# Kernel tuning notes

Hardware: AMD Instinct MI355X
Metric: run time of the kernel (lower is better)

## Reference

```python
import jax, jax.numpy as jnp
import numpy as np

D_MODEL = 1024
NUM_HEADS = 16
HEAD_DIM = D_MODEL // NUM_HEADS
B, T = 4, 2048


def setup_inputs() -> dict:
    key = jax.random.key(0)
    ks = jax.random.split(key, 6)
    s = 1.0 / np.sqrt(D_MODEL)  # ~ nn.Linear init scale
    return {
        "x_q": jax.random.normal(ks[0], (B, T, D_MODEL), jnp.float32),
        "x_kv": jax.random.normal(ks[1], (B, T, D_MODEL), jnp.float32),
        "Wq": jax.random.uniform(ks[2], (D_MODEL, D_MODEL), jnp.float32, -s, s),
        "Wk": jax.random.uniform(ks[3], (D_MODEL, D_MODEL), jnp.float32, -s, s),
        "Wv": jax.random.uniform(ks[4], (D_MODEL, D_MODEL), jnp.float32, -s, s),
        "Wo": jax.random.uniform(ks[5], (D_MODEL, D_MODEL), jnp.float32, -s, s),
    }


def reference(x_q, x_kv, Wq, Wk, Wv, Wo):
    Bq, Tq, C = x_q.shape
    Tk = x_kv.shape[1]
    # torch nn.Linear: y = x @ W.T
    q = (x_q @ Wq.T).reshape(Bq, Tq, NUM_HEADS, HEAD_DIM).transpose(0, 2, 1, 3)
    k = (x_kv @ Wk.T).reshape(Bq, Tk, NUM_HEADS, HEAD_DIM).transpose(0, 2, 1, 3)
    v = (x_kv @ Wv.T).reshape(Bq, Tk, NUM_HEADS, HEAD_DIM).transpose(0, 2, 1, 3)
    scores = jnp.einsum("bhqd,bhkd->bhqk", q, k) / jnp.sqrt(
        jnp.asarray(HEAD_DIM, x_q.dtype)
    )
    causal = jnp.triu(jnp.ones((Tq, Tk), bool), k=1)  # True above diagonal
    scores = jnp.where(causal, -jnp.inf, scores)
    attn = jax.nn.softmax(scores, axis=-1)
    out = jnp.einsum("bhqk,bhkd->bhqd", attn, v)
    out = out.transpose(0, 2, 1, 3).reshape(Bq, Tq, C)
    return out @ Wo.T
```

## Files before the change

kernel.cpp:

```cpp
#include <hip/hip_runtime.h>
#include <stdint.h>

#define T_SEQ 2048
#define NH 16
#define HD 64
#define DM 1024
#define BB 4
#define MROWS (BB * T_SEQ)

#define QSCALE 0.18033688011112042f

typedef __attribute__((ext_vector_type(8))) __bf16 bf16x8;
typedef __attribute__((ext_vector_type(8))) unsigned short u16x8;
typedef __attribute__((ext_vector_type(4))) unsigned short u16x4;
typedef __attribute__((ext_vector_type(4))) float f32x4;

__device__ __forceinline__ unsigned short f2bf(float f) {
  return __builtin_bit_cast(unsigned short, (__bf16)f);
}

__device__ __forceinline__ bf16x8 ld8_f32(const float* __restrict__ p) {
  f32x4 a = *(const f32x4*)p;
  f32x4 b = *(const f32x4*)(p + 4);
  u16x8 u;
#pragma unroll
  for (int i = 0; i < 4; ++i) {
    u[i]     = f2bf(a[i]);
    u[i + 4] = f2bf(b[i]);
  }
  return __builtin_bit_cast(bf16x8, u);
}

__device__ __forceinline__ bf16x8 ld8_bf(const unsigned short* p) {
  return __builtin_bit_cast(bf16x8, *(const u16x8*)p);
}

__device__ __forceinline__ bf16x8 ld8_lds(const unsigned short* p) {
  u16x4 a = *(const u16x4*)p;
  u16x4 b = *(const u16x4*)(p + 4);
  return __builtin_bit_cast(bf16x8,
      __builtin_shufflevector(a, b, 0, 1, 2, 3, 4, 5, 6, 7));
}

__device__ __forceinline__ u16x4 lo4(u16x8 v) {
  return __builtin_shufflevector(v, v, 0, 1, 2, 3);
}
__device__ __forceinline__ u16x4 hi4(u16x8 v) {
  return __builtin_shufflevector(v, v, 4, 5, 6, 7);
}

__device__ __forceinline__ void gload_lds16(const unsigned short* g,
                                            unsigned short* l) {
  __builtin_amdgcn_global_load_lds(
      (const __attribute__((address_space(1))) unsigned int*)g,
      (__attribute__((address_space(3))) unsigned int*)l, 16, 0, 0);
}

__global__ __launch_bounds__(256) void conv_f32_bf16(
    const float* __restrict__ src, unsigned short* __restrict__ dst, int n8) {
  const int i = blockIdx.x * 256 + threadIdx.x;
  if (i < n8)
    *(u16x8*)(dst + (size_t)i * 8) =
        __builtin_bit_cast(u16x8, ld8_f32(src + (size_t)i * 8));
}

__global__ __launch_bounds__(256) void conv_stage1(
    const float* __restrict__ Wk, const float* __restrict__ Wv,
    const float* __restrict__ Wq, const float* __restrict__ Wo,
    const float* __restrict__ xkv, unsigned short* __restrict__ Wkb012,
    unsigned short* __restrict__ Wob, unsigned short* __restrict__ Sx) {
  const int bid = blockIdx.x;
  const int WSEG = (DM * DM / 8) / 256;
  if (bid < 4 * WSEG) {
    const int w = bid >> 9;
    const float* src = (w == 0) ? Wk : (w == 1) ? Wv : (w == 2) ? Wq : Wo;
    unsigned short* dst = (w < 3) ? Wkb012 + (size_t)w * DM * DM : Wob;
    const int i = (bid & (WSEG - 1)) * 256 + threadIdx.x;
    *(u16x8*)(dst + (size_t)i * 8) =
        __builtin_bit_cast(u16x8, ld8_f32(src + (size_t)i * 8));
  } else {
    const int i = (bid - 4 * WSEG) * 256 + threadIdx.x;
    *(u16x8*)(Sx + (size_t)i * 8) =
        __builtin_bit_cast(u16x8, ld8_f32(xkv + (size_t)i * 8));
  }
}

template <int MODE>
__global__ __launch_bounds__(256) void gemm128(
    const unsigned short* __restrict__ A, const unsigned short* __restrict__ B,
    void* __restrict__ Cv, void* __restrict__ Cv2, int M, int N, int K) {
  __shared__ __align__(16) unsigned short As[2][2][128 * 32];
  __shared__ __align__(16) unsigned short Bs[2][2][128 * 32];

  const int t = threadIdx.x;
  const int lane = t & 63, wave = t >> 6;
  const int lin = (int)(blockIdx.x + gridDim.x * blockIdx.y);
  const int nx = N >> 7;
  const int mpx = (M >> 7) >> 3;
  const int xcd = lin & 7, slot = lin >> 3;
  const int m0 = (xcd * mpx + slot / nx) * 128;
  const int n0 = (slot % nx) * 128;

  const int srow = t >> 2;
  const int scol = (t & 3) * 8;
  const unsigned short* ga0 = A + (size_t)(m0 + srow) * K + scol;
  const unsigned short* ga1 = A + (size_t)(m0 + 64 + srow) * K + scol;
  const unsigned short* gb0 = B + (size_t)(n0 + srow) * K + scol;
  const unsigned short* gb1 = B + (size_t)(n0 + 64 + srow) * K + scol;
  const int lo0 = (wave * 16) * 32, lo1 = (64 + wave * 16) * 32;

  const int mw = (wave >> 1) * 64, nw = (wave & 1) * 64;
  const int fr = lane & 15, fq = (lane >> 4) * 8;

  f32x4 acc[4][4];
#pragma unroll
  for (int i = 0; i < 4; ++i)
#pragma unroll
    for (int j = 0; j < 4; ++j) acc[i][j] = (f32x4){0.f, 0.f, 0.f, 0.f};

  auto stage = [&](int buf, int k0) {
    gload_lds16(ga0 + k0,      &As[buf][0][lo0]);
    gload_lds16(ga1 + k0,      &As[buf][0][lo1]);
    gload_lds16(gb0 + k0,      &Bs[buf][0][lo0]);
    gload_lds16(gb1 + k0,      &Bs[buf][0][lo1]);
    gload_lds16(ga0 + k0 + 32, &As[buf][1][lo0]);
    gload_lds16(ga1 + k0 + 32, &As[buf][1][lo1]);
    gload_lds16(gb0 + k0 + 32, &Bs[buf][1][lo0]);
    gload_lds16(gb1 + k0 + 32, &Bs[buf][1][lo1]);
  };

  stage(0, 0);
  __syncthreads();

  const int NT = K >> 6;
  int cur = 0;
  for (int kt = 0; kt < NT; ++kt) {
    if (kt + 1 < NT) stage(cur ^ 1, (kt + 1) << 6);
#pragma unroll
    for (int ks = 0; ks < 2; ++ks) {
      bf16x8 af[4], bfr[4];
#pragma unroll
      for (int i = 0; i < 4; ++i)
        af[i] = ld8_bf(&As[cur][ks][(mw + i * 16 + fr) * 32 + fq]);
#pragma unroll
      for (int j = 0; j < 4; ++j)
        bfr[j] = ld8_bf(&Bs[cur][ks][(nw + j * 16 + fr) * 32 + fq]);
#pragma unroll
      for (int i = 0; i < 4; ++i)
#pragma unroll
        for (int j = 0; j < 4; ++j)
          acc[i][j] = __builtin_amdgcn_mfma_f32_16x16x32_bf16(
              af[i], bfr[j], acc[i][j], 0, 0, 0);
    }
    __syncthreads();
    cur ^= 1;
  }

  const int orow = (lane >> 4) * 4, ocol = lane & 15;
  const bool kv_lo = (MODE == 3) && (n0 < DM);
#pragma unroll
  for (int i = 0; i < 4; ++i)
#pragma unroll
    for (int j = 0; j < 4; ++j) {
      if constexpr (MODE == 2) {
        const int mb = m0 + mw + i * 16 + orow;
        const int n = n0 + nw + j * 16 + ocol;
        u16x4 pk;
#pragma unroll
        for (int r = 0; r < 4; ++r) pk[r] = f2bf(acc[i][j][r]);
        unsigned short* dst = (unsigned short*)Cv +
            ((size_t)((mb >> 11) * NH + (n >> 6)) * HD + (n & 63)) * T_SEQ +
            (mb & 2047);
        *(u16x4*)dst = pk;
      } else if constexpr (MODE == 3) {
        const int mb = m0 + mw + i * 16 + orow;
        const int n = n0 + nw + j * 16 + ocol;
        if (kv_lo) {
#pragma unroll
          for (int r = 0; r < 4; ++r)
            ((unsigned short*)Cv)[(size_t)(mb + r) * DM + n] =
                f2bf(acc[i][j][r]);
        } else {
          const int nv = n - DM;
          u16x4 pk;
#pragma unroll
          for (int r = 0; r < 4; ++r) pk[r] = f2bf(acc[i][j][r]);
          unsigned short* dst = (unsigned short*)Cv2 +
              ((size_t)((mb >> 11) * NH + (nv >> 6)) * HD + (nv & 63)) *
                  T_SEQ +
              (mb & 2047);
          *(u16x4*)dst = pk;
        }
      } else {
#pragma unroll
        for (int r = 0; r < 4; ++r) {
          const size_t idx = (size_t)(m0 + mw + i * 16 + orow + r) * N +
                             (n0 + nw + j * 16 + ocol);
          float v = acc[i][j][r];
          if constexpr (MODE == 4) v *= QSCALE;
          if constexpr (MODE == 1)
            ((float*)Cv)[idx] = v;
          else
            ((unsigned short*)Cv)[idx] = f2bf(v);
        }
      }
    }
}

#define ASTR 68

__global__ __launch_bounds__(256, 2) void attn_flash2(
    const unsigned short* Qw, const unsigned short* __restrict__ Kw,
    const unsigned short* __restrict__ Vt, unsigned short* Ow) {
  __shared__ __align__(16) unsigned short k_lds[2][64][ASTR];
  __shared__ __align__(16) unsigned short vt_lds[2][64][ASTR];
  __shared__ __align__(16) unsigned short p_lds[4][32][ASTR];

  const int tid = threadIdx.x, lane = tid & 63, wave = tid >> 6;
  const int c16 = lane & 15, quad = lane >> 4;
  const int b = blockIdx.z, h = blockIdx.y;
  const int pi = blockIdx.x;
  const int qb0A = (15 - pi) * 128;
  const int qb0B = pi * 128;
  const size_t rkbase = (size_t)b * T_SEQ * DM + (size_t)h * HD;
  const size_t vtbase = (size_t)(b * NH + h) * HD * T_SEQ;

  const int q_loA = qb0A + wave * 32;
  const int q_loB = qb0B + wave * 32;

  bf16x8 qfA[2][2], qfB[2][2];
#pragma unroll
  for (int nf = 0; nf < 2; ++nf) {
    const unsigned short* qpA =
        Qw + rkbase + (size_t)(q_loA + nf * 16 + c16) * DM + quad * 8;
    qfA[nf][0] = ld8_bf(qpA);
    qfA[nf][1] = ld8_bf(qpA + 32);
    const unsigned short* qpB =
        Qw + rkbase + (size_t)(q_loB + nf * 16 + c16) * DM + quad * 8;
    qfB[nf][0] = ld8_bf(qpB);
    qfB[nf][1] = ld8_bf(qpB + 32);
  }

  f32x4 oA[2][4], oB[2][4];
#pragma unroll
  for (int nf = 0; nf < 2; ++nf)
#pragma unroll
    for (int j = 0; j < 4; ++j) {
      oA[nf][j] = (f32x4){0.f, 0.f, 0.f, 0.f};
      oB[nf][j] = (f32x4){0.f, 0.f, 0.f, 0.f};
    }
  float mA[2] = {-3.0e38f, -3.0e38f}, lA[2] = {0.f, 0.f};
  float mB[2] = {-3.0e38f, -3.0e38f}, lB[2] = {0.f, 0.f};

  const int srow = tid >> 2;
  const int scol = (tid & 3) * 16;
  const int ntiles = (qb0A + 191) >> 6;
  const int ntA_w = (q_loA + 95) >> 6;
  const int ntB_w = (q_loB + 95) >> 6;

  const unsigned short* kp0 = Kw + rkbase + (size_t)srow * DM + scol;
  const unsigned short* vp0 = Vt + vtbase + (size_t)srow * T_SEQ + scol;

  auto subtile = [&](const bf16x8 (&qf)[2][2], f32x4 (&o)[2][4],
                     float (&m_r)[2], float (&l_r)[2], const int q_lo,
                     const int kb0, const int bi) {
    f32x4 s[4][2];
    __builtin_amdgcn_s_setprio(1);
#pragma unroll
    for (int mf = 0; mf < 4; ++mf) {
      const unsigned short* kr = &k_lds[bi][mf * 16 + c16][quad * 8];
      const bf16x8 k0 = ld8_lds(kr);
      const bf16x8 k1 = ld8_lds(kr + 32);
#pragma unroll
      for (int nf = 0; nf < 2; ++nf) {
        f32x4 a = {0.f, 0.f, 0.f, 0.f};
        a = __builtin_amdgcn_mfma_f32_16x16x32_bf16(k0, qf[nf][0], a, 0, 0, 0);
        a = __builtin_amdgcn_mfma_f32_16x16x32_bf16(k1, qf[nf][1], a, 0, 0, 0);
        s[mf][nf] = a;
      }
    }
    __builtin_amdgcn_s_setprio(0);
    if (kb0 + 63 > q_lo) {
#pragma unroll
      for (int mf = 0; mf < 4; ++mf) {
        const int key0 = kb0 + mf * 16 + quad * 4;
#pragma unroll
        for (int nf = 0; nf < 2; ++nf) {
          const int qg = q_lo + nf * 16 + c16;
#pragma unroll
          for (int r = 0; r < 4; ++r)
            if (key0 + r > qg) s[mf][nf][r] = -3.0e38f;
        }
      }
    }

#pragma unroll
    for (int nf = 0; nf < 2; ++nf) {
      float mx = -3.0e38f;
#pragma unroll
      for (int mf = 0; mf < 4; ++mf)
#pragma unroll
        for (int r = 0; r < 4; ++r) mx = fmaxf(mx, s[mf][nf][r]);
      mx = fmaxf(mx, __shfl_xor(mx, 16, 64));
      mx = fmaxf(mx, __shfl_xor(mx, 32, 64));
      if (!__all(mx - m_r[nf] <= 8.0f)) {
        const float m_new = fmaxf(m_r[nf], mx);
        const float al = exp2f(m_r[nf] - m_new);
        m_r[nf] = m_new;
        l_r[nf] *= al;
        float alr[4];
#pragma unroll
        for (int r = 0; r < 4; ++r) alr[r] = __shfl(al, quad * 4 + r, 16);
#pragma unroll
        for (int j = 0; j < 4; ++j)
#pragma unroll
          for (int r = 0; r < 4; ++r) o[nf][j][r] *= alr[r];
      }
      float ps = 0.f;
#pragma unroll
      for (int mf = 0; mf < 4; ++mf) {
        u16x4 pk;
#pragma unroll
        for (int r = 0; r < 4; ++r) {
          const float e = exp2f(s[mf][nf][r] - m_r[nf]);
          ps += e;
          pk[r] = f2bf(e);
        }
        *(u16x4*)&p_lds[wave][nf * 16 + c16][mf * 16 + quad * 4] = pk;
      }
      ps += __shfl_xor(ps, 16, 64);
      ps += __shfl_xor(ps, 32, 64);
      l_r[nf] += ps;
    }
    __threadfence_block();

    bf16x8 pf[2][2];
#pragma unroll
    for (int nf = 0; nf < 2; ++nf) {
      const unsigned short* pw = &p_lds[wave][nf * 16 + c16][quad * 8];
      pf[nf][0] = ld8_lds(pw);
      pf[nf][1] = ld8_lds(pw + 32);
    }
    __builtin_amdgcn_s_setprio(1);
#pragma unroll
    for (int j = 0; j < 4; ++j) {
      const unsigned short* vr = &vt_lds[bi][j * 16 + c16][quad * 8];
      const bf16x8 v0 = ld8_lds(vr);
      const bf16x8 v1 = ld8_lds(vr + 32);
#pragma unroll
      for (int nf = 0; nf < 2; ++nf) {
        o[nf][j] = __builtin_amdgcn_mfma_f32_16x16x32_bf16(pf[nf][0], v0,
                                                           o[nf][j], 0, 0, 0);
        o[nf][j] = __builtin_amdgcn_mfma_f32_16x16x32_bf16(pf[nf][1], v1,
                                                           o[nf][j], 0, 0, 0);
      }
    }
    __builtin_amdgcn_s_setprio(0);
  };

  {
    u16x8 ka = *(const u16x8*)kp0;
    u16x8 kc = *(const u16x8*)(kp0 + 8);
    u16x8 va = *(const u16x8*)vp0;
    u16x8 vc = *(const u16x8*)(vp0 + 8);
    *(u16x4*)&k_lds[0][srow][scol]       = lo4(ka);
    *(u16x4*)&k_lds[0][srow][scol + 4]   = hi4(ka);
    *(u16x4*)&k_lds[0][srow][scol + 8]   = lo4(kc);
    *(u16x4*)&k_lds[0][srow][scol + 12]  = hi4(kc);
    *(u16x4*)&vt_lds[0][srow][scol]      = lo4(va);
    *(u16x4*)&vt_lds[0][srow][scol + 4]  = hi4(va);
    *(u16x4*)&vt_lds[0][srow][scol + 8]  = lo4(vc);
    *(u16x4*)&vt_lds[0][srow][scol + 12] = hi4(vc);
  }
  __syncthreads();

  int cur = 0;
  for (int t = 0; t < ntiles; ++t) {
    const int kb0 = t * 64;
    const bool pf = (t + 1 < ntiles);
    u16x8 ka, kc, va, vc;
    if (pf) {
      const unsigned short* kp = kp0 + (size_t)(kb0 + 64) * DM;
      ka = *(const u16x8*)kp;
      kc = *(const u16x8*)(kp + 8);
      const unsigned short* vp = vp0 + (kb0 + 64);
      va = *(const u16x8*)vp;
      vc = *(const u16x8*)(vp + 8);
    }
    if (t < ntA_w) subtile(qfA, oA, mA, lA, q_loA, kb0, cur);
    if (t < ntB_w) subtile(qfB, oB, mB, lB, q_loB, kb0, cur);
    if (pf) {
      const int nb = cur ^ 1;
      *(u16x4*)&k_lds[nb][srow][scol]       = lo4(ka);
      *(u16x4*)&k_lds[nb][srow][scol + 4]   = hi4(ka);
      *(u16x4*)&k_lds[nb][srow][scol + 8]   = lo4(kc);
      *(u16x4*)&k_lds[nb][srow][scol + 12]  = hi4(kc);
      *(u16x4*)&vt_lds[nb][srow][scol]      = lo4(va);
      *(u16x4*)&vt_lds[nb][srow][scol + 4]  = hi4(va);
      *(u16x4*)&vt_lds[nb][srow][scol + 8]  = lo4(vc);
      *(u16x4*)&vt_lds[nb][srow][scol + 12] = hi4(vc);
      __syncthreads();
      cur = nb;
    }
  }

  auto epi = [&](f32x4 (&o)[2][4], float (&l_r)[2], const int q_lo) {
#pragma unroll
    for (int nf = 0; nf < 2; ++nf)
#pragma unroll
      for (int r = 0; r < 4; ++r) {
        const int qg = q_lo + nf * 16 + quad * 4 + r;
        const float inv = 1.0f / __shfl(l_r[nf], quad * 4 + r, 16);
        unsigned short* orow = Ow + rkbase + (size_t)qg * DM;
#pragma unroll
        for (int j = 0; j < 4; ++j)
          orow[j * 16 + c16] = f2bf(o[nf][j][r] * inv);
      }
  };
  epi(oA, lA, q_loA);
  epi(oB, lB, q_loB);
}

extern "C" void kernel_launch(void* const* d_in, const int* in_sizes, int n_in,
                              void* d_out, int out_size, void* d_ws, size_t ws_size,
                              hipStream_t stream) {
  const float* x_q  = (const float*)d_in[0];
  const float* x_kv = (const float*)d_in[1];
  const float* Wq   = (const float*)d_in[2];
  const float* Wk   = (const float*)d_in[3];
  const float* Wv   = (const float*)d_in[4];
  const float* Wo   = (const float*)d_in[5];
  float* out = (float*)d_out;

  unsigned short* scr  = (unsigned short*)d_out;
  unsigned short* Sx   = scr;
  unsigned short* Wk_b = scr + (size_t)MROWS * DM;
  unsigned short* Wv_b = Wk_b + (size_t)DM * DM;
  unsigned short* Wq_b = Wv_b + (size_t)DM * DM;

  unsigned short* qb   = (unsigned short*)d_ws;
  unsigned short* kb   = qb + (size_t)MROWS * DM;
  unsigned short* vtb  = kb + (size_t)MROWS * DM;
  unsigned short* Wo_b = vtb + (size_t)MROWS * DM;

  const int nW8 = DM * DM / 8;
  const int nX8 = MROWS * DM / 8;
  (void)Wv_b;

  conv_stage1<<<4 * (nW8 / 256) + nX8 / 256, 256, 0, stream>>>(
      Wk, Wv, Wq, Wo, x_kv, Wk_b, Wo_b, Sx);

  gemm128<3><<<dim3(2 * DM / 128, MROWS / 128), 256, 0, stream>>>(
      Sx, Wk_b, kb, vtb, MROWS, 2 * DM, DM);
  conv_f32_bf16<<<nX8 / 256, 256, 0, stream>>>(x_q, Sx, nX8);
  gemm128<4><<<dim3(DM / 128, MROWS / 128), 256, 0, stream>>>(
      Sx, Wq_b, qb, nullptr, MROWS, DM, DM);
  attn_flash2<<<dim3(8, NH, BB), 256, 0, stream>>>(qb, kb, vtb, qb);
  gemm128<1><<<dim3(DM / 128, MROWS / 128), 256, 0, stream>>>(
      qb, Wo_b, out, nullptr, MROWS, DM, DM);
}
```

Measured before the change: 294.5 us.

## Halve attention query tile per block to raise occupancy, drop K/V double buffering

Each attention block now handles 64 query rows per side, 16 per wave instead of 32, and the grid doubles to 16 blocks along x. Register and LDS use drop, since K/V shared buffers are single-buffered and the P scratch is halved, and the launch bound goes from 2 to 4 blocks per CU to allow more resident waves. In exchange, the software prefetch overlap of global K/V loads is gone, each tile load now sits between two barriers, and K/V tiles are reloaded by twice as many blocks. The unused MODE 2 GEMM epilogue is also removed.

```diff
diff --git a/kernel.cpp b/kernel.cpp
--- a/kernel.cpp
+++ b/kernel.cpp
@@ -162,19 +162,9 @@
   for (int i = 0; i < 4; ++i)
 #pragma unroll
     for (int j = 0; j < 4; ++j) {
-      if constexpr (MODE == 2) {
-        const int mb = m0 + mw + i * 16 + orow;
-        const int n = n0 + nw + j * 16 + ocol;
-        u16x4 pk;
-#pragma unroll
-        for (int r = 0; r < 4; ++r) pk[r] = f2bf(acc[i][j][r]);
-        unsigned short* dst = (unsigned short*)Cv +
-            ((size_t)((mb >> 11) * NH + (n >> 6)) * HD + (n & 63)) * T_SEQ +
-            (mb & 2047);
-        *(u16x4*)dst = pk;
-      } else if constexpr (MODE == 3) {
-        const int mb = m0 + mw + i * 16 + orow;
-        const int n = n0 + nw + j * 16 + ocol;
+      const int mb = m0 + mw + i * 16 + orow;
+      const int n = n0 + nw + j * 16 + ocol;
+      if constexpr (MODE == 3) {
         if (kv_lo) {
 #pragma unroll
           for (int r = 0; r < 4; ++r)
@@ -194,8 +184,7 @@
       } else {
 #pragma unroll
         for (int r = 0; r < 4; ++r) {
-          const size_t idx = (size_t)(m0 + mw + i * 16 + orow + r) * N +
-                             (n0 + nw + j * 16 + ocol);
+          const size_t idx = (size_t)(mb + r) * N + n;
           float v = acc[i][j][r];
           if constexpr (MODE == 4) v *= QSCALE;
           if constexpr (MODE == 1)
@@ -209,216 +198,174 @@
 
 #define ASTR 68
 
-__global__ __launch_bounds__(256, 2) void attn_flash2(
+__global__ __launch_bounds__(256, 4) void attn_flash2(
     const unsigned short* Qw, const unsigned short* __restrict__ Kw,
     const unsigned short* __restrict__ Vt, unsigned short* Ow) {
-  __shared__ __align__(16) unsigned short k_lds[2][64][ASTR];
-  __shared__ __align__(16) unsigned short vt_lds[2][64][ASTR];
-  __shared__ __align__(16) unsigned short p_lds[4][32][ASTR];
+  __shared__ __align__(16) unsigned short k_lds[64][ASTR];
+  __shared__ __align__(16) unsigned short vt_lds[64][ASTR];
+  __shared__ __align__(16) unsigned short p_lds[4][16][ASTR];
 
   const int tid = threadIdx.x, lane = tid & 63, wave = tid >> 6;
   const int c16 = lane & 15, quad = lane >> 4;
   const int b = blockIdx.z, h = blockIdx.y;
-  const int pi = blockIdx.x;
-  const int qb0A = (15 - pi) * 128;
-  const int qb0B = pi * 128;
+  const int pi = blockIdx.x >> 1;
+  const int half = blockIdx.x & 1;
+  const int qb0A = (15 - pi) * 128 + half * 64;
+  const int qb0B = pi * 128 + half * 64;
   const size_t rkbase = (size_t)b * T_SEQ * DM + (size_t)h * HD;
   const size_t vtbase = (size_t)(b * NH + h) * HD * T_SEQ;
 
-  const int q_loA = qb0A + wave * 32;
-  const int q_loB = qb0B + wave * 32;
-
-  bf16x8 qfA[2][2], qfB[2][2];
-#pragma unroll
-  for (int nf = 0; nf < 2; ++nf) {
+  const int q_loA = qb0A + wave * 16;
+  const int q_loB = qb0B + wave * 16;
+
+  bf16x8 qfA[2], qfB[2];
+  {
     const unsigned short* qpA =
-        Qw + rkbase + (size_t)(q_loA + nf * 16 + c16) * DM + quad * 8;
-    qfA[nf][0] = ld8_bf(qpA);
-    qfA[nf][1] = ld8_bf(qpA + 32);
+        Qw + rkbase + (size_t)(q_loA + c16) * DM + quad * 8;
+    qfA[0] = ld8_bf(qpA);
+    qfA[1] = ld8_bf(qpA + 32);
     const unsigned short* qpB =
-        Qw + rkbase + (size_t)(q_loB + nf * 16 + c16) * DM + quad * 8;
-    qfB[nf][0] = ld8_bf(qpB);
-    qfB[nf][1] = ld8_bf(qpB + 32);
-  }
-
-  f32x4 oA[2][4], oB[2][4];
-#pragma unroll
-  for (int nf = 0; nf < 2; ++nf)
-#pragma unroll
-    for (int j = 0; j < 4; ++j) {
-      oA[nf][j] = (f32x4){0.f, 0.f, 0.f, 0.f};
-      oB[nf][j] = (f32x4){0.f, 0.f, 0.f, 0.f};
-    }
-  float mA[2] = {-3.0e38f, -3.0e38f}, lA[2] = {0.f, 0.f};
-  float mB[2] = {-3.0e38f, -3.0e38f}, lB[2] = {0.f, 0.f};
+        Qw + rkbase + (size_t)(q_loB + c16) * DM + quad * 8;
+    qfB[0] = ld8_bf(qpB);
+    qfB[1] = ld8_bf(qpB + 32);
+  }
+
+  f32x4 oA[4], oB[4];
+#pragma unroll
+  for (int j = 0; j < 4; ++j) {
+    oA[j] = (f32x4){0.f, 0.f, 0.f, 0.f};
+    oB[j] = (f32x4){0.f, 0.f, 0.f, 0.f};
+  }
+  float mA = -3.0e38f, lAr = 0.f;
+  float mB = -3.0e38f, lBr = 0.f;
 
   const int srow = tid >> 2;
   const int scol = (tid & 3) * 16;
-  const int ntiles = (qb0A + 191) >> 6;
-  const int ntA_w = (q_loA + 95) >> 6;
-  const int ntB_w = (q_loB + 95) >> 6;
+  const int ntiles = (qb0A + 127) >> 6;
+  const int ntA_w = (q_loA + 79) >> 6;
+  const int ntB_w = (q_loB + 79) >> 6;
 
   const unsigned short* kp0 = Kw + rkbase + (size_t)srow * DM + scol;
   const unsigned short* vp0 = Vt + vtbase + (size_t)srow * T_SEQ + scol;
 
-  auto subtile = [&](const bf16x8 (&qf)[2][2], f32x4 (&o)[2][4],
-                     float (&m_r)[2], float (&l_r)[2], const int q_lo,
-                     const int kb0, const int bi) {
-    f32x4 s[4][2];
+  auto subtile = [&](const bf16x8 (&qf)[2], f32x4 (&o)[4], float& m_r,
+                     float& l_r, const int q_lo, const int kb0) {
+    f32x4 s[4];
     __builtin_amdgcn_s_setprio(1);
 #pragma unroll
     for (int mf = 0; mf < 4; ++mf) {
-      const unsigned short* kr = &k_lds[bi][mf * 16 + c16][quad * 8];
+      const unsigned short* kr = &k_lds[mf * 16 + c16][quad * 8];
       const bf16x8 k0 = ld8_lds(kr);
       const bf16x8 k1 = ld8_lds(kr + 32);
-#pragma unroll
-      for (int nf = 0; nf < 2; ++nf) {
-        f32x4 a = {0.f, 0.f, 0.f, 0.f};
-        a = __builtin_amdgcn_mfma_f32_16x16x32_bf16(k0, qf[nf][0], a, 0, 0, 0);
-        a = __builtin_amdgcn_mfma_f32_16x16x32_bf16(k1, qf[nf][1], a, 0, 0, 0);
-        s[mf][nf] = a;
-      }
+      f32x4 a = {0.f, 0.f, 0.f, 0.f};
+      a = __builtin_amdgcn_mfma_f32_16x16x32_bf16(k0, qf[0], a, 0, 0, 0);
+      a = __builtin_amdgcn_mfma_f32_16x16x32_bf16(k1, qf[1], a, 0, 0, 0);
+      s[mf] = a;
     }
     __builtin_amdgcn_s_setprio(0);
     if (kb0 + 63 > q_lo) {
+      const int qg = q_lo + c16;
 #pragma unroll
       for (int mf = 0; mf < 4; ++mf) {
         const int key0 = kb0 + mf * 16 + quad * 4;
 #pragma unroll
-        for (int nf = 0; nf < 2; ++nf) {
-          const int qg = q_lo + nf * 16 + c16;
-#pragma unroll
-          for (int r = 0; r < 4; ++r)
-            if (key0 + r > qg) s[mf][nf][r] = -3.0e38f;
-        }
+        for (int r = 0; r < 4; ++r)
+          if (key0 + r > qg) s[mf][r] = -3.0e38f;
       }
     }
 
-#pragma unroll
-    for (int nf = 0; nf < 2; ++nf) {
-      float mx = -3.0e38f;
-#pragma unroll
-      for (int mf = 0; mf < 4; ++mf)
-#pragma unroll
-        for (int r = 0; r < 4; ++r) mx = fmaxf(mx, s[mf][nf][r]);
-      mx = fmaxf(mx, __shfl_xor(mx, 16, 64));
-      mx = fmaxf(mx, __shfl_xor(mx, 32, 64));
-      if (!__all(mx - m_r[nf] <= 8.0f)) {
-        const float m_new = fmaxf(m_r[nf], mx);
-        const float al = exp2f(m_r[nf] - m_new);
-        m_r[nf] = m_new;
-        l_r[nf] *= al;
-        float alr[4];
-#pragma unroll
-        for (int r = 0; r < 4; ++r) alr[r] = __shfl(al, quad * 4 + r, 16);
-#pragma unroll
-        for (int j = 0; j < 4; ++j)
-#pragma unroll
-          for (int r = 0; r < 4; ++r) o[nf][j][r] *= alr[r];
+    float mx = -3.0e38f;
+#pragma unroll
+    for (int mf = 0; mf < 4; ++mf)
+#pragma unroll
+      for (int r = 0; r < 4; ++r) mx = fmaxf(mx, s[mf][r]);
+    mx = fmaxf(mx, __shfl_xor(mx, 16, 64));
+    mx = fmaxf(mx, __shfl_xor(mx, 32, 64));
+    if (!__all(mx - m_r <= 8.0f)) {
+      const float m_new = fmaxf(m_r, mx);
+      const float al = exp2f(m_r - m_new);
+      m_r = m_new;
+      l_r *= al;
+      float alr[4];
+#pragma unroll
+      for (int r = 0; r < 4; ++r) alr[r] = __shfl(al, quad * 4 + r, 16);
+#pragma unroll
+      for (int j = 0; j < 4; ++j)
+#pragma unroll
+        for (int r = 0; r < 4; ++r) o[j][r] *= alr[r];
+    }
+    float ps = 0.f;
+#pragma unroll
+    for (int mf = 0; mf < 4; ++mf) {
+      u16x4 pk;
+#pragma unroll
+      for (int r = 0; r < 4; ++r) {
+        const float e = exp2f(s[mf][r] - m_r);
+        ps += e;
+        pk[r] = f2bf(e);
       }
-      float ps = 0.f;
-#pragma unroll
-      for (int mf = 0; mf < 4; ++mf) {
-        u16x4 pk;
-#pragma unroll
-        for (int r = 0; r < 4; ++r) {
-          const float e = exp2f(s[mf][nf][r] - m_r[nf]);
-          ps += e;
-          pk[r] = f2bf(e);
-        }
-        *(u16x4*)&p_lds[wave][nf * 16 + c16][mf * 16 + quad * 4] = pk;
-      }
-      ps += __shfl_xor(ps, 16, 64);
-      ps += __shfl_xor(ps, 32, 64);
-      l_r[nf] += ps;
-    }
+      *(u16x4*)&p_lds[wave][c16][mf * 16 + quad * 4] = pk;
+    }
+    ps += __shfl_xor(ps, 16, 64);
+    ps += __shfl_xor(ps, 32, 64);
+    l_r += ps;
     __threadfence_block();
 
-    bf16x8 pf[2][2];
-#pragma unroll
-    for (int nf = 0; nf < 2; ++nf) {
-      const unsigned short* pw = &p_lds[wave][nf * 16 + c16][quad * 8];
-      pf[nf][0] = ld8_lds(pw);
-      pf[nf][1] = ld8_lds(pw + 32);
+    bf16x8 pf0, pf1;
+    {
+      const unsigned short* pw = &p_lds[wave][c16][quad * 8];
+      pf0 = ld8_lds(pw);
+      pf1 = ld8_lds(pw + 32);
     }
     __builtin_amdgcn_s_setprio(1);
 #pragma unroll
     for (int j = 0; j < 4; ++j) {
-      const unsigned short* vr = &vt_lds[bi][j * 16 + c16][quad * 8];
+      const unsigned short* vr = &vt_lds[j * 16 + c16][quad * 8];
       const bf16x8 v0 = ld8_lds(vr);
       const bf16x8 v1 = ld8_lds(vr + 32);
-#pragma unroll
-      for (int nf = 0; nf < 2; ++nf) {
-        o[nf][j] = __builtin_amdgcn_mfma_f32_16x16x32_bf16(pf[nf][0], v0,
-                                                           o[nf][j], 0, 0, 0);
-        o[nf][j] = __builtin_amdgcn_mfma_f32_16x16x32_bf16(pf[nf][1], v1,
-                                                           o[nf][j], 0, 0, 0);
-      }
+      o[j] = __builtin_amdgcn_mfma_f32_16x16x32_bf16(pf0, v0, o[j], 0, 0, 0);
+      o[j] = __builtin_amdgcn_mfma_f32_16x16x32_bf16(pf1, v1, o[j], 0, 0, 0);
     }
     __builtin_amdgcn_s_setprio(0);
   };
 
-  {
-    u16x8 ka = *(const u16x8*)kp0;
-    u16x8 kc = *(const u16x8*)(kp0 + 8);
-    u16x8 va = *(const u16x8*)vp0;
-    u16x8 vc = *(const u16x8*)(vp0 + 8);
-    *(u16x4*)&k_lds[0][srow][scol]       = lo4(ka);
-    *(u16x4*)&k_lds[0][srow][scol + 4]   = hi4(ka);
-    *(u16x4*)&k_lds[0][srow][scol + 8]   = lo4(kc);
-    *(u16x4*)&k_lds[0][srow][scol + 12]  = hi4(kc);
-    *(u16x4*)&vt_lds[0][srow][scol]      = lo4(va);
-    *(u16x4*)&vt_lds[0][srow][scol + 4]  = hi4(va);
-    *(u16x4*)&vt_lds[0][srow][scol + 8]  = lo4(vc);
-    *(u16x4*)&vt_lds[0][srow][scol + 12] = hi4(vc);
-  }
-  __syncthreads();
-
-  int cur = 0;
   for (int t = 0; t < ntiles; ++t) {
     const int kb0 = t * 64;
-    const bool pf = (t + 1 < ntiles);
-    u16x8 ka, kc, va, vc;
-    if (pf) {
-      const unsigned short* kp = kp0 + (size_t)(kb0 + 64) * DM;
-      ka = *(const u16x8*)kp;
-      kc = *(const u16x8*)(kp + 8);
-      const unsigned short* vp = vp0 + (kb0 + 64);
-      va = *(const u16x8*)vp;
-      vc = *(const u16x8*)(vp + 8);
-    }
-    if (t < ntA_w) subtile(qfA, oA, mA, lA, q_loA, kb0, cur);
-    if (t < ntB_w) subtile(qfB, oB, mB, lB, q_loB, kb0, cur);
-    if (pf) {
-      const int nb = cur ^ 1;
-      *(u16x4*)&k_lds[nb][srow][scol]       = lo4(ka);
-      *(u16x4*)&k_lds[nb][srow][scol + 4]   = hi4(ka);
-      *(u16x4*)&k_lds[nb][srow][scol + 8]   = lo4(kc);
-      *(u16x4*)&k_lds[nb][srow][scol + 12]  = hi4(kc);
-      *(u16x4*)&vt_lds[nb][srow][scol]      = lo4(va);
-      *(u16x4*)&vt_lds[nb][srow][scol + 4]  = hi4(va);
-      *(u16x4*)&vt_lds[nb][srow][scol + 8]  = lo4(vc);
-      *(u16x4*)&vt_lds[nb][srow][scol + 12] = hi4(vc);
-      __syncthreads();
-      cur = nb;
-    }
-  }
-
-  auto epi = [&](f32x4 (&o)[2][4], float (&l_r)[2], const int q_lo) {
-#pragma unroll
-    for (int nf = 0; nf < 2; ++nf)
-#pragma unroll
-      for (int r = 0; r < 4; ++r) {
-        const int qg = q_lo + nf * 16 + quad * 4 + r;
-        const float inv = 1.0f / __shfl(l_r[nf], quad * 4 + r, 16);
-        unsigned short* orow = Ow + rkbase + (size_t)qg * DM;
-#pragma unroll
-        for (int j = 0; j < 4; ++j)
-          orow[j * 16 + c16] = f2bf(o[nf][j][r] * inv);
-      }
+    __syncthreads();
+    {
+      const unsigned short* kp = kp0 + (size_t)kb0 * DM;
+      u16x8 ka = *(const u16x8*)kp;
+      u16x8 kc = *(const u16x8*)(kp + 8);
+      const unsigned short* vp = vp0 + kb0;
+      u16x8 va = *(const u16x8*)vp;
+      u16x8 vc = *(const u16x8*)(vp + 8);
+      *(u16x4*)&k_lds[srow][scol]       = lo4(ka);
+      *(u16x4*)&k_lds[srow][scol + 4]   = hi4(ka);
+      *(u16x4*)&k_lds[srow][scol + 8]   = lo4(kc);
+      *(u16x4*)&k_lds[srow][scol + 12]  = hi4(kc);
+      *(u16x4*)&vt_lds[srow][scol]      = lo4(va);
+      *(u16x4*)&vt_lds[srow][scol + 4]  = hi4(va);
+      *(u16x4*)&vt_lds[srow][scol + 8]  = lo4(vc);
+      *(u16x4*)&vt_lds[srow][scol + 12] = hi4(vc);
+    }
+    __syncthreads();
+    if (t < ntA_w) subtile(qfA, oA, mA, lAr, q_loA, kb0);
+    if (t < ntB_w) subtile(qfB, oB, mB, lBr, q_loB, kb0);
+  }
+
+  auto epi = [&](f32x4 (&o)[4], float l_r, const int q_lo) {
+#pragma unroll
+    for (int r = 0; r < 4; ++r) {
+      const int qg = q_lo + quad * 4 + r;
+      const float inv = 1.0f / __shfl(l_r, quad * 4 + r, 16);
+      unsigned short* orow = Ow + rkbase + (size_t)qg * DM;
+#pragma unroll
+      for (int j = 0; j < 4; ++j)
+        orow[j * 16 + c16] = f2bf(o[j][r] * inv);
+    }
   };
-  epi(oA, lA, q_loA);
-  epi(oB, lB, q_loB);
+  epi(oA, lAr, q_loA);
+  epi(oB, lBr, q_loB);
 }
 
 extern "C" void kernel_launch(void* const* d_in, const int* in_sizes, int n_in,
@@ -455,7 +402,7 @@
   conv_f32_bf16<<<nX8 / 256, 256, 0, stream>>>(x_q, Sx, nX8);
   gemm128<4><<<dim3(DM / 128, MROWS / 128), 256, 0, stream>>>(
       Sx, Wq_b, qb, nullptr, MROWS, DM, DM);
-  attn_flash2<<<dim3(8, NH, BB), 256, 0, stream>>>(qb, kb, vtb, qb);
+  attn_flash2<<<dim3(16, NH, BB), 256, 0, stream>>>(qb, kb, vtb, qb);
   gemm128<1><<<dim3(DM / 128, MROWS / 128), 256, 0, stream>>>(
       qb, Wo_b, out, nullptr, MROWS, DM, DM);
 }
```

New measurement: 298.8 us. Within noise of the previous version (+1.5%).
